# Optimization experiments

Measured on AMD Instinct MI355X. Metric: run time of the kernel, lower is better.

## Reference

```python
import jax, jax.numpy as jnp
import numpy as np

B, N, E, H = 2, 512, 128, 256
IN_DIM = 3 * E + 1


def setup_inputs() -> dict:
    key = jax.random.key(0)
    ks = jax.random.split(key, 9)
    node_embed = jax.random.normal(ks[0], (B, N, E), dtype=jnp.float32)
    problems = jax.random.uniform(ks[1], (B, N, 4), dtype=jnp.float32)
    euclid = jax.random.uniform(ks[2], (B, N, N), dtype=jnp.float32)
    euclid = 0.5 * (euclid + jnp.swapaxes(euclid, 1, 2))  # symmetric, realistic
    s = 0.02
    W1 = s * jax.random.normal(ks[3], (IN_DIM, H), dtype=jnp.float32)
    b1 = jnp.zeros((H,), jnp.float32)
    W2 = s * jax.random.normal(ks[4], (H, H), dtype=jnp.float32)
    b2 = jnp.zeros((H,), jnp.float32)
    W3 = s * jax.random.normal(ks[5], (H, 1), dtype=jnp.float32)
    b3 = jnp.zeros((1,), jnp.float32)
    return {"node_embed": node_embed, "problems": problems,
            "euclid_distance_matrix": euclid,
            "W1": W1, "b1": b1, "W2": W2, "b2": b2, "W3": W3, "b3": b3}


def _forward(node_embed, euclid, W1, b1, W2, b2, W3, b3):
    b, n, e = node_embed.shape
    hi = jnp.broadcast_to(node_embed[:, :, None, :], (b, n, n, e))
    hj = jnp.broadcast_to(node_embed[:, None, :, :], (b, n, n, e))
    habs = jnp.abs(node_embed[:, :, None, :] - node_embed[:, None, :, :])
    x = jnp.concatenate([hi, hj, habs, euclid[..., None]], axis=-1)  # (B,N,N,3E+1)
    h = jax.nn.relu(jnp.einsum('bijf,fh->bijh', x, W1) + b1)
    h = jax.nn.relu(jnp.einsum('bijh,hg->bijg', h, W2) + b2)
    pred = (jnp.einsum('bijh,ho->bijo', h, W3) + b3)[..., 0]  # (B,N,N)
    pred = 0.5 * (pred + jnp.swapaxes(pred, 1, 2))
    pred = pred * (1.0 - jnp.eye(n, dtype=pred.dtype))  # zero diagonal
    return pred


def reference(node_embed, problems, euclid_distance_matrix, W1, b1, W2, b2, W3, b3):
    # euclid_distance_matrix provided, so `problems` fallback path is unused
    return _forward(node_embed, euclid_distance_matrix, W1, b1, W2, b2, W3, b3)
```

## Files before the change

kernel.cpp:

```cpp
#include <hip/hip_runtime.h>
#include <hip/hip_bf16.h>


#define BN 512
#define EE 128
#define HH 256

typedef __attribute__((ext_vector_type(8)))  short short8;
typedef __attribute__((ext_vector_type(4)))  short short4v;
typedef __attribute__((ext_vector_type(16))) float f32x16;
typedef __attribute__((ext_vector_type(4)))  float f32x4;

static __device__ __forceinline__ unsigned short f2bf(float f) {
    __bf16 h = (__bf16)f;
    return __builtin_bit_cast(unsigned short, h);
}
static __device__ __forceinline__ f32x16 zero16() {
    f32x16 v;
    #pragma unroll
    for (int i = 0; i < 16; ++i) v[i] = 0.f;
    return v;
}
#define MFMA(a, b, c) __builtin_amdgcn_mfma_f32_32x32x16_bf16((a), (b), (c), 0, 0, 0)

__global__ void prep(const float* __restrict__ node, const float* __restrict__ W1,
                     const float* __restrict__ W2, const float* __restrict__ b1,
                     float* __restrict__ PA,
                     unsigned short* __restrict__ w1c_p, unsigned short* __restrict__ w1b_p,
                     unsigned short* __restrict__ w2_p,  unsigned short* __restrict__ w1d_f) {
    int blk = blockIdx.x;
    if (blk < 256) {
        int idx = blk * 256 + threadIdx.x;
        {
            int t = idx & 7, l = (idx >> 3) & 63, mt = (idx >> 9) & 7, kb = idx >> 12;
            int k = kb * 16 + (l >> 5) * 8 + t, m = mt * 32 + (l & 31);
            w2_p[idx] = f2bf(W2[k * HH + m]);
            if (idx < 32768) {
                w1c_p[idx] = f2bf(W1[(2 * EE + k) * HH + m]);
                w1b_p[idx] = f2bf(W1[(EE + k) * HH + m]);
            }
        }
        if (idx < 4096) {
            int t = idx & 7, l = (idx >> 3) & 63, mt = idx >> 9;
            int m = mt * 32 + (l & 31);
            bool nz = (t == 0 && l < 32);
            w1d_f[idx] = nz ? f2bf(W1[(3 * EE) * HH + m]) : (unsigned short)0;
        }
    } else {
        int bi = blk - 256;
        int h = threadIdx.x;
        const float* nd = node + (size_t)bi * EE;
        float sa = b1[h];
        #pragma unroll 8
        for (int e = 0; e < EE; ++e) sa += nd[e] * W1[e * HH + h];
        PA[bi * HH + h] = sa;
    }
}

__global__ __launch_bounds__(256, 2) void edge_main(
    const float* __restrict__ node, const float* __restrict__ euclid,
    const float* __restrict__ W3, const float* __restrict__ b3,
    const float* __restrict__ b2v, const float* __restrict__ PA,
    const unsigned short* __restrict__ w1c_p, const unsigned short* __restrict__ w1b_p,
    const unsigned short* __restrict__ w2_p,  const unsigned short* __restrict__ w1d_f,
    float* __restrict__ out)
{
    __shared__ __align__(16) unsigned short lds_buf[2 * 128 * 136];
    __shared__ float pp[512];

    const int jt = blockIdx.x, i = blockIdx.y, b = blockIdx.z;
    const int jbase = jt * 128;
    const int tid = threadIdx.x, wave = tid >> 6, lane = tid & 63;
    const int m0 = lane & 31, q = lane >> 5;

    unsigned short* ldsD  = lds_buf;
    unsigned short* ldsHJ = lds_buf + 128 * 136;
    unsigned short* ldsH1 = lds_buf;

    {
        int row = tid >> 1, half = tid & 1;
        const f32x4* nj = (const f32x4*)(node + ((size_t)b * BN + jbase + row) * EE);
        const f32x4* hv = (const f32x4*)(node + ((size_t)b * BN + i) * EE);
        #pragma unroll
        for (int g = 0; g < 8; ++g) {
            int c0 = half * 16 + g * 2;
            f32x4 a0 = nj[c0], a1 = nj[c0 + 1];
            f32x4 h0 = hv[c0], h1v = hv[c0 + 1];
            short8 pd, ph;
            #pragma unroll
            for (int u = 0; u < 4; ++u) {
                pd[u]     = (short)f2bf(fabsf(a0[u] - h0[u]));
                pd[4 + u] = (short)f2bf(fabsf(a1[u] - h1v[u]));
                ph[u]     = (short)f2bf(a0[u]);
                ph[4 + u] = (short)f2bf(a1[u]);
            }
            int off = row * 136 + half * 64 + g * 8;
            *(short8*)&ldsD[off]  = pd;
            *(short8*)&ldsHJ[off] = ph;
        }
    }
    __syncthreads();

    f32x16 acc[2][4];
    #pragma unroll
    for (int mt = 0; mt < 2; ++mt)
        #pragma unroll
        for (int nt = 0; nt < 4; ++nt) acc[mt][nt] = zero16();
    {
        const short8* wc = (const short8*)w1c_p;
        const short8* wb = (const short8*)w1b_p;
        const int mtg = wave * 2;
        #pragma unroll
        for (int kb = 0; kb < 8; ++kb) {
            short8 ac0 = wc[(kb * 8 + mtg + 0) * 64 + lane];
            short8 ac1 = wc[(kb * 8 + mtg + 1) * 64 + lane];
            short8 ab0 = wb[(kb * 8 + mtg + 0) * 64 + lane];
            short8 ab1 = wb[(kb * 8 + mtg + 1) * 64 + lane];
            #pragma unroll
            for (int nt = 0; nt < 4; ++nt) {
                int off = (nt * 32 + m0) * 136 + kb * 16 + q * 8;
                short8 bD  = *(const short8*)&ldsD[off];
                short8 bHJ = *(const short8*)&ldsHJ[off];
                acc[0][nt] = MFMA(ac0, bD, acc[0][nt]);
                acc[1][nt] = MFMA(ac1, bD, acc[1][nt]);
                acc[0][nt] = MFMA(ab0, bHJ, acc[0][nt]);
                acc[1][nt] = MFMA(ab1, bHJ, acc[1][nt]);
            }
        }
        const float* erow = euclid + ((size_t)b * BN + i) * BN + jbase;
        short8 aw0 = ((const short8*)w1d_f)[(mtg + 0) * 64 + lane];
        short8 aw1 = ((const short8*)w1d_f)[(mtg + 1) * 64 + lane];
        #pragma unroll
        for (int nt = 0; nt < 4; ++nt) {
            short8 be;
            #pragma unroll
            for (int u = 0; u < 8; ++u) be[u] = 0;
            if (lane < 32) be[0] = (short)f2bf(erow[nt * 32 + m0]);
            acc[0][nt] = MFMA(aw0, be, acc[0][nt]);
            acc[1][nt] = MFMA(aw1, be, acc[1][nt]);
        }
    }
    __syncthreads();

    {
        const float* paB = PA + ((size_t)b * BN + i) * HH;
        #pragma unroll
        for (int mt = 0; mt < 2; ++mt) {
            #pragma unroll
            for (int rg = 0; rg < 4; ++rg) {
                int f0 = wave * 64 + mt * 32 + rg * 8;
                f32x4 plo = *(const f32x4*)&paB[f0];
                f32x4 phi = *(const f32x4*)&paB[f0 + 4];
                f32x4 pav;
                #pragma unroll
                for (int u = 0; u < 4; ++u) pav[u] = q ? phi[u] : plo[u];
                #pragma unroll
                for (int nt = 0; nt < 4; ++nt) {
                    short4v w;
                    #pragma unroll
                    for (int u = 0; u < 4; ++u) {
                        float v = acc[mt][nt][rg * 4 + u] + pav[u];
                        v = v > 0.f ? v : 0.f;
                        w[u] = (short)f2bf(v);
                    }
                    *(short4v*)&ldsH1[(nt * 32 + m0) * 264 + f0 + 4 * q] = w;
                }
            }
        }
    }
    __syncthreads();

    f32x16 c2[2][4];
    #pragma unroll
    for (int mt = 0; mt < 2; ++mt)
        #pragma unroll
        for (int nt = 0; nt < 4; ++nt) c2[mt][nt] = zero16();
    {
        const short8* w2f = (const short8*)w2_p;
        const int mtg = wave * 2;
        #pragma unroll
        for (int kb = 0; kb < 16; ++kb) {
            short8 a0 = w2f[(kb * 8 + mtg + 0) * 64 + lane];
            short8 a1 = w2f[(kb * 8 + mtg + 1) * 64 + lane];
            #pragma unroll
            for (int nt = 0; nt < 4; ++nt) {
                short8 bh = *(const short8*)&ldsH1[(nt * 32 + m0) * 264 + kb * 16 + q * 8];
                c2[0][nt] = MFMA(a0, bh, c2[0][nt]);
                c2[1][nt] = MFMA(a1, bh, c2[1][nt]);
            }
        }
    }

    {
        float s[4] = {0.f, 0.f, 0.f, 0.f};
        #pragma unroll
        for (int mt = 0; mt < 2; ++mt) {
            #pragma unroll
            for (int rg = 0; rg < 4; ++rg) {
                int f0 = wave * 64 + mt * 32 + rg * 8;
                f32x4 blo = *(const f32x4*)&b2v[f0];
                f32x4 bhi = *(const f32x4*)&b2v[f0 + 4];
                f32x4 wlo = *(const f32x4*)&W3[f0];
                f32x4 whi = *(const f32x4*)&W3[f0 + 4];
                #pragma unroll
                for (int u = 0; u < 4; ++u) {
                    float bb = q ? bhi[u] : blo[u];
                    float ww = q ? whi[u] : wlo[u];
                    #pragma unroll
                    for (int nt = 0; nt < 4; ++nt) {
                        float h2 = c2[mt][nt][rg * 4 + u] + bb;
                        h2 = h2 > 0.f ? h2 : 0.f;
                        s[nt] += h2 * ww;
                    }
                }
            }
        }
        #pragma unroll
        for (int nt = 0; nt < 4; ++nt)
            s[nt] += __shfl_xor(s[nt], 32, 64);
        if (lane < 32) {
            #pragma unroll
            for (int nt = 0; nt < 4; ++nt)
                pp[wave * 128 + nt * 32 + lane] = s[nt];
        }
    }
    __syncthreads();
    if (tid < 128) {
        float v = pp[tid] + pp[128 + tid] + pp[256 + tid] + pp[384 + tid] + b3[0];
        out[((size_t)b * BN + i) * BN + jbase + tid] = v;
    }
}

__global__ void symmetrize(float* __restrict__ out) {
    int b = blockIdx.z, ti = blockIdx.y, tj = blockIdx.x;
    if (tj < ti) return;
    int i = ti * 32 + threadIdx.y, j = tj * 32 + threadIdx.x;
    float* p = out + (size_t)b * BN * BN;
    if (i == j) { p[(size_t)i * BN + j] = 0.f; return; }
    if (j < i) return;
    float a = p[(size_t)i * BN + j];
    float c = p[(size_t)j * BN + i];
    float v = 0.5f * (a + c);
    p[(size_t)i * BN + j] = v;
    p[(size_t)j * BN + i] = v;
}

extern "C" void kernel_launch(void* const* d_in, const int* in_sizes, int n_in,
                              void* d_out, int out_size, void* d_ws, size_t ws_size,
                              hipStream_t stream) {
    const float* node   = (const float*)d_in[0];
    const float* euclid = (const float*)d_in[2];
    const float* W1     = (const float*)d_in[3];
    const float* b1     = (const float*)d_in[4];
    const float* W2     = (const float*)d_in[5];
    const float* b2     = (const float*)d_in[6];
    const float* W3     = (const float*)d_in[7];
    const float* b3     = (const float*)d_in[8];
    float* out = (float*)d_out;

    char* ws = (char*)d_ws;
    float*          PA    = (float*)ws;
    unsigned short* w1c_p = (unsigned short*)(ws + (1u << 20));
    unsigned short* w1b_p = (unsigned short*)(ws + (1u << 20) + 65536);
    unsigned short* w2_p  = (unsigned short*)(ws + (1u << 20) + 131072);
    unsigned short* w1d_f = (unsigned short*)(ws + (1u << 20) + 262144);

    prep<<<1280, 256, 0, stream>>>(node, W1, W2, b1, PA, w1c_p, w1b_p, w2_p, w1d_f);
    edge_main<<<dim3(BN / 128, BN, 2), 256, 0, stream>>>(
        node, euclid, W3, b3, b2, PA, w1c_p, w1b_p, w2_p, w1d_f, out);
    symmetrize<<<dim3(BN / 32, BN / 32, 2), dim3(32, 32), 0, stream>>>(out);
}
```

Measured before the change: 236.1 us.

## Persistent 512-thread blocks loop over 16 rows with double-buffered diff tiles

The edge kernel now launches 256 blocks of 512 threads, and each block iterates over 16 consecutive i rows for a fixed 128-column j tile. The hj bf16 tile is staged in LDS once per block. The |hi-hj| tile for the next row is computed into a second LDS buffer during the current row's first-layer MFMAs, and the output store for the previous row is deferred into the next iteration. The aim is to amortise per-block staging and launch overhead and to overlap global loads with compute. In exchange the grid is much smaller, LDS use per block is larger, and each wave handles a 2x2 tile subset.

```diff
diff --git a/kernel.cpp b/kernel.cpp
--- a/kernel.cpp
+++ b/kernel.cpp
@@ -57,7 +57,7 @@
     }
 }
 
-__global__ __launch_bounds__(256, 2) void edge_main(
+__global__ __launch_bounds__(512, 2) void edge_main(
     const float* __restrict__ node, const float* __restrict__ euclid,
     const float* __restrict__ W3, const float* __restrict__ b3,
     const float* __restrict__ b2v, const float* __restrict__ PA,
@@ -65,27 +65,36 @@
     const unsigned short* __restrict__ w2_p,  const unsigned short* __restrict__ w1d_f,
     float* __restrict__ out)
 {
-    __shared__ __align__(16) unsigned short lds_buf[2 * 128 * 136];
+    __shared__ __align__(16) unsigned short Rd[2][128 * 136];
+    __shared__ __align__(16) unsigned short Rh[128 * 136];
+    __shared__ __align__(16) unsigned short Rhj[128 * 136];
     __shared__ float pp[512];
 
-    const int jt = blockIdx.x, i = blockIdx.y, b = blockIdx.z;
-    const int jbase = jt * 128;
+    const int wg = blockIdx.x;
+    const int b = wg >> 7, jt = (wg >> 5) & 3, ig = wg & 31;
+    const int jbase = jt * 128, i0 = ig * 16;
     const int tid = threadIdx.x, wave = tid >> 6, lane = tid & 63;
     const int m0 = lane & 31, q = lane >> 5;
-
-    unsigned short* ldsD  = lds_buf;
-    unsigned short* ldsHJ = lds_buf + 128 * 136;
-    unsigned short* ldsH1 = lds_buf;
+    const int mt2 = wave & 3, ntg = wave >> 2;
+    const int nt0 = 2 * ntg, nt1 = 2 * ntg + 1;
+
+    const int brow = tid >> 2, bq4 = tid & 3;
+    const f32x4* njp = (const f32x4*)(node + ((size_t)b * BN + jbase + brow) * EE);
+
+    const float b3v = b3[0];
+    const short8 aw0 = ((const short8*)w1d_f)[(2 * mt2 + 0) * 64 + lane];
+    const short8 aw1 = ((const short8*)w1d_f)[(2 * mt2 + 1) * 64 + lane];
+    const short8* wc  = (const short8*)w1c_p;
+    const short8* wb  = (const short8*)w1b_p;
+    const short8* w2f = (const short8*)w2_p;
 
     {
-        int row = tid >> 1, half = tid & 1;
-        const f32x4* nj = (const f32x4*)(node + ((size_t)b * BN + jbase + row) * EE);
-        const f32x4* hv = (const f32x4*)(node + ((size_t)b * BN + i) * EE);
+        const f32x4* hv = (const f32x4*)(node + ((size_t)b * BN + i0) * EE);
         #pragma unroll
-        for (int g = 0; g < 8; ++g) {
-            int c0 = half * 16 + g * 2;
-            f32x4 a0 = nj[c0], a1 = nj[c0 + 1];
-            f32x4 h0 = hv[c0], h1v = hv[c0 + 1];
+        for (int k = 0; k < 4; ++k) {
+            int c0 = bq4 * 8 + k * 2;
+            f32x4 a0 = njp[c0], a1 = njp[c0 + 1];
+            f32x4 h0 = hv[c0],  h1v = hv[c0 + 1];
             short8 pd, ph;
             #pragma unroll
             for (int u = 0; u < 4; ++u) {
@@ -94,140 +103,154 @@
                 ph[u]     = (short)f2bf(a0[u]);
                 ph[4 + u] = (short)f2bf(a1[u]);
             }
-            int off = row * 136 + half * 64 + g * 8;
-            *(short8*)&ldsD[off]  = pd;
-            *(short8*)&ldsHJ[off] = ph;
+            int off = brow * 136 + bq4 * 32 + k * 8;
+            *(short8*)&Rd[0][off]  = pd;
+            *(short8*)&Rhj[off]    = ph;
         }
     }
     __syncthreads();
 
-    f32x16 acc[2][4];
-    #pragma unroll
-    for (int mt = 0; mt < 2; ++mt)
-        #pragma unroll
-        for (int nt = 0; nt < 4; ++nt) acc[mt][nt] = zero16();
-    {
-        const short8* wc = (const short8*)w1c_p;
-        const short8* wb = (const short8*)w1b_p;
-        const int mtg = wave * 2;
-        #pragma unroll
-        for (int kb = 0; kb < 8; ++kb) {
-            short8 ac0 = wc[(kb * 8 + mtg + 0) * 64 + lane];
-            short8 ac1 = wc[(kb * 8 + mtg + 1) * 64 + lane];
-            short8 ab0 = wb[(kb * 8 + mtg + 0) * 64 + lane];
-            short8 ab1 = wb[(kb * 8 + mtg + 1) * 64 + lane];
-            #pragma unroll
-            for (int nt = 0; nt < 4; ++nt) {
-                int off = (nt * 32 + m0) * 136 + kb * 16 + q * 8;
-                short8 bD  = *(const short8*)&ldsD[off];
-                short8 bHJ = *(const short8*)&ldsHJ[off];
-                acc[0][nt] = MFMA(ac0, bD, acc[0][nt]);
-                acc[1][nt] = MFMA(ac1, bD, acc[1][nt]);
-                acc[0][nt] = MFMA(ab0, bHJ, acc[0][nt]);
-                acc[1][nt] = MFMA(ab1, bHJ, acc[1][nt]);
-            }
-        }
-        const float* erow = euclid + ((size_t)b * BN + i) * BN + jbase;
-        short8 aw0 = ((const short8*)w1d_f)[(mtg + 0) * 64 + lane];
-        short8 aw1 = ((const short8*)w1d_f)[(mtg + 1) * 64 + lane];
-        #pragma unroll
-        for (int nt = 0; nt < 4; ++nt) {
-            short8 be;
-            #pragma unroll
-            for (int u = 0; u < 8; ++u) be[u] = 0;
-            if (lane < 32) be[0] = (short)f2bf(erow[nt * 32 + m0]);
-            acc[0][nt] = MFMA(aw0, be, acc[0][nt]);
-            acc[1][nt] = MFMA(aw1, be, acc[1][nt]);
-        }
-    }
-    __syncthreads();
-
-    {
-        const float* paB = PA + ((size_t)b * BN + i) * HH;
-        #pragma unroll
-        for (int mt = 0; mt < 2; ++mt) {
-            #pragma unroll
-            for (int rg = 0; rg < 4; ++rg) {
-                int f0 = wave * 64 + mt * 32 + rg * 8;
-                f32x4 plo = *(const f32x4*)&paB[f0];
-                f32x4 phi = *(const f32x4*)&paB[f0 + 4];
-                f32x4 pav;
-                #pragma unroll
-                for (int u = 0; u < 4; ++u) pav[u] = q ? phi[u] : plo[u];
-                #pragma unroll
-                for (int nt = 0; nt < 4; ++nt) {
-                    short4v w;
+    #pragma unroll 1
+    for (int tt = 0; tt < 16; ++tt) {
+        const int i = i0 + tt;
+        unsigned short* Dcur = Rd[tt & 1];
+        unsigned short* Dnxt = Rd[(tt + 1) & 1];
+
+        if (tt > 0 && tid < 128) {
+            float v = pp[tid * 4] + pp[tid * 4 + 1] + pp[tid * 4 + 2] + pp[tid * 4 + 3] + b3v;
+            out[((size_t)b * BN + (i - 1)) * BN + jbase + tid] = v;
+        }
+
+        f32x16 acc[2][2];
+        acc[0][0] = zero16(); acc[0][1] = zero16();
+        acc[1][0] = zero16(); acc[1][1] = zero16();
+        {
+            const f32x4* hvn = (const f32x4*)(node + ((size_t)b * BN + i + 1) * EE);
+            #pragma unroll
+            for (int kb = 0; kb < 8; ++kb) {
+                if (kb < 4 && tt < 15) {
+                    int c0 = bq4 * 8 + kb * 2;
+                    f32x4 a0 = njp[c0], a1 = njp[c0 + 1];
+                    f32x4 h0 = hvn[c0], h1v = hvn[c0 + 1];
+                    short8 pd;
                     #pragma unroll
                     for (int u = 0; u < 4; ++u) {
-                        float v = acc[mt][nt][rg * 4 + u] + pav[u];
-                        v = v > 0.f ? v : 0.f;
-                        w[u] = (short)f2bf(v);
+                        pd[u]     = (short)f2bf(fabsf(a0[u] - h0[u]));
+                        pd[4 + u] = (short)f2bf(fabsf(a1[u] - h1v[u]));
                     }
-                    *(short4v*)&ldsH1[(nt * 32 + m0) * 264 + f0 + 4 * q] = w;
+                    *(short8*)&Dnxt[brow * 136 + bq4 * 32 + kb * 8] = pd;
                 }
-            }
-        }
-    }
-    __syncthreads();
-
-    f32x16 c2[2][4];
-    #pragma unroll
-    for (int mt = 0; mt < 2; ++mt)
-        #pragma unroll
-        for (int nt = 0; nt < 4; ++nt) c2[mt][nt] = zero16();
-    {
-        const short8* w2f = (const short8*)w2_p;
-        const int mtg = wave * 2;
-        #pragma unroll
-        for (int kb = 0; kb < 16; ++kb) {
-            short8 a0 = w2f[(kb * 8 + mtg + 0) * 64 + lane];
-            short8 a1 = w2f[(kb * 8 + mtg + 1) * 64 + lane];
-            #pragma unroll
-            for (int nt = 0; nt < 4; ++nt) {
-                short8 bh = *(const short8*)&ldsH1[(nt * 32 + m0) * 264 + kb * 16 + q * 8];
-                c2[0][nt] = MFMA(a0, bh, c2[0][nt]);
-                c2[1][nt] = MFMA(a1, bh, c2[1][nt]);
-            }
-        }
-    }
-
-    {
-        float s[4] = {0.f, 0.f, 0.f, 0.f};
-        #pragma unroll
-        for (int mt = 0; mt < 2; ++mt) {
-            #pragma unroll
-            for (int rg = 0; rg < 4; ++rg) {
-                int f0 = wave * 64 + mt * 32 + rg * 8;
-                f32x4 blo = *(const f32x4*)&b2v[f0];
-                f32x4 bhi = *(const f32x4*)&b2v[f0 + 4];
-                f32x4 wlo = *(const f32x4*)&W3[f0];
-                f32x4 whi = *(const f32x4*)&W3[f0 + 4];
+                short8 ac0 = wc[(kb * 8 + 2 * mt2 + 0) * 64 + lane];
+                short8 ac1 = wc[(kb * 8 + 2 * mt2 + 1) * 64 + lane];
+                short8 ab0 = wb[(kb * 8 + 2 * mt2 + 0) * 64 + lane];
+                short8 ab1 = wb[(kb * 8 + 2 * mt2 + 1) * 64 + lane];
+                int o0 = (nt0 * 32 + m0) * 136 + kb * 16 + q * 8;
+                int o1 = (nt1 * 32 + m0) * 136 + kb * 16 + q * 8;
+                short8 bD0 = *(const short8*)&Dcur[o0];
+                short8 bD1 = *(const short8*)&Dcur[o1];
+                short8 bH0 = *(const short8*)&Rhj[o0];
+                short8 bH1 = *(const short8*)&Rhj[o1];
+                acc[0][0] = MFMA(ac0, bD0, acc[0][0]);
+                acc[1][0] = MFMA(ac1, bD0, acc[1][0]);
+                acc[0][1] = MFMA(ac0, bD1, acc[0][1]);
+                acc[1][1] = MFMA(ac1, bD1, acc[1][1]);
+                acc[0][0] = MFMA(ab0, bH0, acc[0][0]);
+                acc[1][0] = MFMA(ab1, bH0, acc[1][0]);
+                acc[0][1] = MFMA(ab0, bH1, acc[0][1]);
+                acc[1][1] = MFMA(ab1, bH1, acc[1][1]);
+            }
+            const float* erow = euclid + ((size_t)b * BN + i) * BN + jbase;
+            #pragma unroll
+            for (int nt2 = 0; nt2 < 2; ++nt2) {
+                short8 be;
                 #pragma unroll
-                for (int u = 0; u < 4; ++u) {
-                    float bb = q ? bhi[u] : blo[u];
-                    float ww = q ? whi[u] : wlo[u];
+                for (int u = 0; u < 8; ++u) be[u] = 0;
+                if (lane < 32) be[0] = (short)f2bf(erow[(nt0 + nt2) * 32 + m0]);
+                acc[0][nt2] = MFMA(aw0, be, acc[0][nt2]);
+                acc[1][nt2] = MFMA(aw1, be, acc[1][nt2]);
+            }
+        }
+        __syncthreads();
+
+        {
+            const float* paB = PA + ((size_t)b * BN + i) * HH;
+            unsigned short* base = (mt2 < 2) ? Dcur : Rh;
+            #pragma unroll
+            for (int mtl = 0; mtl < 2; ++mtl) {
+                int mt = 2 * mt2 + mtl;
+                #pragma unroll
+                for (int rg = 0; rg < 4; ++rg) {
+                    int f0 = mt * 32 + rg * 8 + 4 * q;
+                    f32x4 pav = *(const f32x4*)&paB[f0];
+                    int lc = f0 & 127;
                     #pragma unroll
-                    for (int nt = 0; nt < 4; ++nt) {
-                        float h2 = c2[mt][nt][rg * 4 + u] + bb;
-                        h2 = h2 > 0.f ? h2 : 0.f;
-                        s[nt] += h2 * ww;
+                    for (int nt2 = 0; nt2 < 2; ++nt2) {
+                        short4v w;
+                        #pragma unroll
+                        for (int u = 0; u < 4; ++u) {
+                            float v = acc[mtl][nt2][rg * 4 + u] + pav[u];
+                            v = v > 0.f ? v : 0.f;
+                            w[u] = (short)f2bf(v);
+                        }
+                        *(short4v*)&base[((nt0 + nt2) * 32 + m0) * 136 + lc] = w;
                     }
                 }
             }
         }
-        #pragma unroll
-        for (int nt = 0; nt < 4; ++nt)
-            s[nt] += __shfl_xor(s[nt], 32, 64);
-        if (lane < 32) {
-            #pragma unroll
-            for (int nt = 0; nt < 4; ++nt)
-                pp[wave * 128 + nt * 32 + lane] = s[nt];
-        }
-    }
-    __syncthreads();
+        __syncthreads();
+
+        f32x16 c2[2][2];
+        c2[0][0] = zero16(); c2[0][1] = zero16();
+        c2[1][0] = zero16(); c2[1][1] = zero16();
+        {
+            #pragma unroll
+            for (int kb = 0; kb < 16; ++kb) {
+                const unsigned short* src = (kb < 8) ? Dcur : Rh;
+                short8 a0 = w2f[(kb * 8 + 2 * mt2 + 0) * 64 + lane];
+                short8 a1 = w2f[(kb * 8 + 2 * mt2 + 1) * 64 + lane];
+                int o0 = (nt0 * 32 + m0) * 136 + (kb & 7) * 16 + q * 8;
+                int o1 = (nt1 * 32 + m0) * 136 + (kb & 7) * 16 + q * 8;
+                short8 bh0 = *(const short8*)&src[o0];
+                short8 bh1 = *(const short8*)&src[o1];
+                c2[0][0] = MFMA(a0, bh0, c2[0][0]);
+                c2[1][0] = MFMA(a1, bh0, c2[1][0]);
+                c2[0][1] = MFMA(a0, bh1, c2[0][1]);
+                c2[1][1] = MFMA(a1, bh1, c2[1][1]);
+            }
+        }
+        {
+            float s0 = 0.f, s1 = 0.f;
+            #pragma unroll
+            for (int mtl = 0; mtl < 2; ++mtl) {
+                #pragma unroll
+                for (int rg = 0; rg < 4; ++rg) {
+                    int f0 = (2 * mt2 + mtl) * 32 + rg * 8 + 4 * q;
+                    f32x4 bb = *(const f32x4*)&b2v[f0];
+                    f32x4 ww = *(const f32x4*)&W3[f0];
+                    #pragma unroll
+                    for (int u = 0; u < 4; ++u) {
+                        float h2a = c2[mtl][0][rg * 4 + u] + bb[u];
+                        h2a = h2a > 0.f ? h2a : 0.f;
+                        s0 += h2a * ww[u];
+                        float h2b = c2[mtl][1][rg * 4 + u] + bb[u];
+                        h2b = h2b > 0.f ? h2b : 0.f;
+                        s1 += h2b * ww[u];
+                    }
+                }
+            }
+            s0 += __shfl_xor(s0, 32, 64);
+            s1 += __shfl_xor(s1, 32, 64);
+            if (lane < 32) {
+                pp[(nt0 * 32 + lane) * 4 + mt2] = s0;
+                pp[(nt1 * 32 + lane) * 4 + mt2] = s1;
+            }
+        }
+        __syncthreads();
+    }
+
     if (tid < 128) {
-        float v = pp[tid] + pp[128 + tid] + pp[256 + tid] + pp[384 + tid] + b3[0];
-        out[((size_t)b * BN + i) * BN + jbase + tid] = v;
+        float v = pp[tid * 4] + pp[tid * 4 + 1] + pp[tid * 4 + 2] + pp[tid * 4 + 3] + b3v;
+        out[((size_t)b * BN + (i0 + 15)) * BN + jbase + tid] = v;
     }
 }
 
@@ -266,7 +289,7 @@
     unsigned short* w1d_f = (unsigned short*)(ws + (1u << 20) + 262144);
 
     prep<<<1280, 256, 0, stream>>>(node, W1, W2, b1, PA, w1c_p, w1b_p, w2_p, w1d_f);
-    edge_main<<<dim3(BN / 128, BN, 2), 256, 0, stream>>>(
+    edge_main<<<256, 512, 0, stream>>>(
         node, euclid, W3, b3, b2, PA, w1c_p, w1b_p, w2_p, w1d_f, out);
     symmetrize<<<dim3(BN / 32, BN / 32, 2), dim3(32, 32), 0, stream>>>(out);
 }
```

Result: slower. 455.9 us (+93.1%).

## Precompute hj·W1 per node and loop eight i rows per block

Applied to the files above, without the earlier changes.

The hj contribution to layer 1 is now computed once per node in the prep kernel as PB, a per-node projection, and loaded to initialise the accumulators. This removes half of the layer-1 MFMAs and the hj LDS staging. The edge kernel becomes a 512-block grid where each block processes eight consecutive i rows in a loop. This is meant to amortise per-block setup and weight fetches, at the cost of fewer blocks in flight and extra fp32 global reads of PB per iteration. An empty asm barrier stops the compiler from hoisting the loop-invariant loads and blowing up register use.

```diff
diff --git a/kernel.cpp b/kernel.cpp
--- a/kernel.cpp
+++ b/kernel.cpp
@@ -25,9 +25,9 @@
 
 __global__ void prep(const float* __restrict__ node, const float* __restrict__ W1,
                      const float* __restrict__ W2, const float* __restrict__ b1,
-                     float* __restrict__ PA,
-                     unsigned short* __restrict__ w1c_p, unsigned short* __restrict__ w1b_p,
-                     unsigned short* __restrict__ w2_p,  unsigned short* __restrict__ w1d_f) {
+                     float* __restrict__ PA, float* __restrict__ PB,
+                     unsigned short* __restrict__ w1c_p, unsigned short* __restrict__ w2_p,
+                     unsigned short* __restrict__ w1d_f) {
     int blk = blockIdx.x;
     if (blk < 256) {
         int idx = blk * 256 + threadIdx.x;
@@ -35,10 +35,8 @@
             int t = idx & 7, l = (idx >> 3) & 63, mt = (idx >> 9) & 7, kb = idx >> 12;
             int k = kb * 16 + (l >> 5) * 8 + t, m = mt * 32 + (l & 31);
             w2_p[idx] = f2bf(W2[k * HH + m]);
-            if (idx < 32768) {
+            if (idx < 32768)
                 w1c_p[idx] = f2bf(W1[(2 * EE + k) * HH + m]);
-                w1b_p[idx] = f2bf(W1[(EE + k) * HH + m]);
-            }
         }
         if (idx < 4096) {
             int t = idx & 7, l = (idx >> 3) & 63, mt = idx >> 9;
@@ -50,10 +48,15 @@
         int bi = blk - 256;
         int h = threadIdx.x;
         const float* nd = node + (size_t)bi * EE;
-        float sa = b1[h];
-        #pragma unroll 8
-        for (int e = 0; e < EE; ++e) sa += nd[e] * W1[e * HH + h];
+        float sa = b1[h], sb = 0.f;
+        #pragma unroll 4
+        for (int e = 0; e < EE; ++e) {
+            float x = nd[e];
+            sa += x * W1[e * HH + h];
+            sb += x * W1[(EE + e) * HH + h];
+        }
         PA[bi * HH + h] = sa;
+        PB[bi * HH + h] = sb;
     }
 }
 
@@ -61,173 +64,179 @@
     const float* __restrict__ node, const float* __restrict__ euclid,
     const float* __restrict__ W3, const float* __restrict__ b3,
     const float* __restrict__ b2v, const float* __restrict__ PA,
-    const unsigned short* __restrict__ w1c_p, const unsigned short* __restrict__ w1b_p,
-    const unsigned short* __restrict__ w2_p,  const unsigned short* __restrict__ w1d_f,
+    const float* __restrict__ PB,
+    const unsigned short* __restrict__ w1c_p, const unsigned short* __restrict__ w2_p,
+    const unsigned short* __restrict__ w1d_f,
     float* __restrict__ out)
 {
-    __shared__ __align__(16) unsigned short lds_buf[2 * 128 * 136];
+    __shared__ __align__(16) unsigned short lds_buf[128 * 264];
     __shared__ float pp[512];
 
-    const int jt = blockIdx.x, i = blockIdx.y, b = blockIdx.z;
-    const int jbase = jt * 128;
+    const int id = blockIdx.x;
+    const int ig = id >> 3, b = (id >> 2) & 1, jt = id & 3;
+    const int jbase = jt * 128, i0 = ig * 8;
     const int tid = threadIdx.x, wave = tid >> 6, lane = tid & 63;
     const int m0 = lane & 31, q = lane >> 5;
-
-    unsigned short* ldsD  = lds_buf;
-    unsigned short* ldsHJ = lds_buf + 128 * 136;
-    unsigned short* ldsH1 = lds_buf;
-
-    {
-        int row = tid >> 1, half = tid & 1;
-        const f32x4* nj = (const f32x4*)(node + ((size_t)b * BN + jbase + row) * EE);
-        const f32x4* hv = (const f32x4*)(node + ((size_t)b * BN + i) * EE);
+    const int brow = tid >> 1, bhalf = tid & 1;
+
+    const float b3v = b3[0];
+    const short8 aw0 = ((const short8*)w1d_f)[(wave * 2 + 0) * 64 + lane];
+    const short8 aw1 = ((const short8*)w1d_f)[(wave * 2 + 1) * 64 + lane];
+    const float* pbBase = PB + ((size_t)b * BN + jbase) * HH;
+    int prow[4];
+    #pragma unroll
+    for (int nt = 0; nt < 4; ++nt) prow[nt] = (nt * 32 + m0) * HH;
+
+    #pragma unroll 1
+    for (int tt = 0; tt < 8; ++tt) {
+        const int i = i0 + tt;
+        size_t z = 0;
+        asm volatile("" : "+s"(z));
+        const short8* wcT = (const short8*)w1c_p + z;
+        const short8* w2T = (const short8*)w2_p + z;
+        const float*  pbT = pbBase + z;
+        const f32x4*  njT = (const f32x4*)(node + ((size_t)b * BN + jbase + brow) * EE) + z;
+        const float*  b2T = b2v + z;
+        const float*  w3T = W3 + z;
+
+        f32x16 acc[2][4];
         #pragma unroll
-        for (int g = 0; g < 8; ++g) {
-            int c0 = half * 16 + g * 2;
-            f32x4 a0 = nj[c0], a1 = nj[c0 + 1];
-            f32x4 h0 = hv[c0], h1v = hv[c0 + 1];
-            short8 pd, ph;
-            #pragma unroll
-            for (int u = 0; u < 4; ++u) {
-                pd[u]     = (short)f2bf(fabsf(a0[u] - h0[u]));
-                pd[4 + u] = (short)f2bf(fabsf(a1[u] - h1v[u]));
-                ph[u]     = (short)f2bf(a0[u]);
-                ph[4 + u] = (short)f2bf(a1[u]);
-            }
-            int off = row * 136 + half * 64 + g * 8;
-            *(short8*)&ldsD[off]  = pd;
-            *(short8*)&ldsHJ[off] = ph;
-        }
-    }
-    __syncthreads();
-
-    f32x16 acc[2][4];
-    #pragma unroll
-    for (int mt = 0; mt < 2; ++mt)
+        for (int mtl = 0; mtl < 2; ++mtl) {
+            #pragma unroll
+            for (int rg = 0; rg < 4; ++rg) {
+                int f0 = wave * 64 + mtl * 32 + rg * 8 + 4 * q;
+                #pragma unroll
+                for (int nt = 0; nt < 4; ++nt) {
+                    f32x4 v = *(const f32x4*)&pbT[prow[nt] + f0];
+                    #pragma unroll
+                    for (int u = 0; u < 4; ++u) acc[mtl][nt][rg * 4 + u] = v[u];
+                }
+            }
+        }
+        const float* erow = euclid + ((size_t)b * BN + i) * BN + jbase;
+        float ev[4];
         #pragma unroll
-        for (int nt = 0; nt < 4; ++nt) acc[mt][nt] = zero16();
-    {
-        const short8* wc = (const short8*)w1c_p;
-        const short8* wb = (const short8*)w1b_p;
-        const int mtg = wave * 2;
+        for (int nt = 0; nt < 4; ++nt) ev[nt] = erow[nt * 32 + m0];
+
+        {
+            const f32x4* hv = (const f32x4*)(node + ((size_t)b * BN + i) * EE);
+            #pragma unroll
+            for (int g = 0; g < 8; ++g) {
+                int c0 = bhalf * 16 + g * 2;
+                f32x4 a0 = njT[c0], a1 = njT[c0 + 1];
+                f32x4 h0 = hv[c0],  h1v = hv[c0 + 1];
+                short8 pd;
+                #pragma unroll
+                for (int u = 0; u < 4; ++u) {
+                    pd[u]     = (short)f2bf(fabsf(a0[u] - h0[u]));
+                    pd[4 + u] = (short)f2bf(fabsf(a1[u] - h1v[u]));
+                }
+                *(short8*)&lds_buf[brow * 136 + bhalf * 64 + g * 8] = pd;
+            }
+        }
+        __syncthreads();
+
+        {
+            #pragma unroll
+            for (int kb = 0; kb < 8; ++kb) {
+                short8 ac0 = wcT[(kb * 8 + wave * 2 + 0) * 64 + lane];
+                short8 ac1 = wcT[(kb * 8 + wave * 2 + 1) * 64 + lane];
+                #pragma unroll
+                for (int nt = 0; nt < 4; ++nt) {
+                    short8 bD = *(const short8*)&lds_buf[(nt * 32 + m0) * 136 + kb * 16 + q * 8];
+                    acc[0][nt] = MFMA(ac0, bD, acc[0][nt]);
+                    acc[1][nt] = MFMA(ac1, bD, acc[1][nt]);
+                }
+            }
+            #pragma unroll
+            for (int nt = 0; nt < 4; ++nt) {
+                short8 be;
+                #pragma unroll
+                for (int u = 0; u < 8; ++u) be[u] = 0;
+                if (lane < 32) be[0] = (short)f2bf(ev[nt]);
+                acc[0][nt] = MFMA(aw0, be, acc[0][nt]);
+                acc[1][nt] = MFMA(aw1, be, acc[1][nt]);
+            }
+        }
+        __syncthreads();
+
+        {
+            const float* paB = PA + ((size_t)b * BN + i) * HH;
+            #pragma unroll
+            for (int mtl = 0; mtl < 2; ++mtl) {
+                #pragma unroll
+                for (int rg = 0; rg < 4; ++rg) {
+                    int f0 = wave * 64 + mtl * 32 + rg * 8 + 4 * q;
+                    f32x4 pav = *(const f32x4*)&paB[f0];
+                    #pragma unroll
+                    for (int nt = 0; nt < 4; ++nt) {
+                        short4v w;
+                        #pragma unroll
+                        for (int u = 0; u < 4; ++u) {
+                            float v = acc[mtl][nt][rg * 4 + u] + pav[u];
+                            v = v > 0.f ? v : 0.f;
+                            w[u] = (short)f2bf(v);
+                        }
+                        *(short4v*)&lds_buf[(nt * 32 + m0) * 264 + f0] = w;
+                    }
+                }
+            }
+        }
+        __syncthreads();
+
+        f32x16 c2[2][4];
         #pragma unroll
-        for (int kb = 0; kb < 8; ++kb) {
-            short8 ac0 = wc[(kb * 8 + mtg + 0) * 64 + lane];
-            short8 ac1 = wc[(kb * 8 + mtg + 1) * 64 + lane];
-            short8 ab0 = wb[(kb * 8 + mtg + 0) * 64 + lane];
-            short8 ab1 = wb[(kb * 8 + mtg + 1) * 64 + lane];
-            #pragma unroll
-            for (int nt = 0; nt < 4; ++nt) {
-                int off = (nt * 32 + m0) * 136 + kb * 16 + q * 8;
-                short8 bD  = *(const short8*)&ldsD[off];
-                short8 bHJ = *(const short8*)&ldsHJ[off];
-                acc[0][nt] = MFMA(ac0, bD, acc[0][nt]);
-                acc[1][nt] = MFMA(ac1, bD, acc[1][nt]);
-                acc[0][nt] = MFMA(ab0, bHJ, acc[0][nt]);
-                acc[1][nt] = MFMA(ab1, bHJ, acc[1][nt]);
-            }
-        }
-        const float* erow = euclid + ((size_t)b * BN + i) * BN + jbase;
-        short8 aw0 = ((const short8*)w1d_f)[(mtg + 0) * 64 + lane];
-        short8 aw1 = ((const short8*)w1d_f)[(mtg + 1) * 64 + lane];
-        #pragma unroll
-        for (int nt = 0; nt < 4; ++nt) {
-            short8 be;
-            #pragma unroll
-            for (int u = 0; u < 8; ++u) be[u] = 0;
-            if (lane < 32) be[0] = (short)f2bf(erow[nt * 32 + m0]);
-            acc[0][nt] = MFMA(aw0, be, acc[0][nt]);
-            acc[1][nt] = MFMA(aw1, be, acc[1][nt]);
-        }
-    }
-    __syncthreads();
-
-    {
-        const float* paB = PA + ((size_t)b * BN + i) * HH;
-        #pragma unroll
-        for (int mt = 0; mt < 2; ++mt) {
-            #pragma unroll
-            for (int rg = 0; rg < 4; ++rg) {
-                int f0 = wave * 64 + mt * 32 + rg * 8;
-                f32x4 plo = *(const f32x4*)&paB[f0];
-                f32x4 phi = *(const f32x4*)&paB[f0 + 4];
-                f32x4 pav;
-                #pragma unroll
-                for (int u = 0; u < 4; ++u) pav[u] = q ? phi[u] : plo[u];
+        for (int mtl = 0; mtl < 2; ++mtl)
+            #pragma unroll
+            for (int nt = 0; nt < 4; ++nt) c2[mtl][nt] = zero16();
+        {
+            #pragma unroll
+            for (int kb = 0; kb < 16; ++kb) {
+                short8 a0 = w2T[(kb * 8 + wave * 2 + 0) * 64 + lane];
+                short8 a1 = w2T[(kb * 8 + wave * 2 + 1) * 64 + lane];
                 #pragma unroll
                 for (int nt = 0; nt < 4; ++nt) {
-                    short4v w;
+                    short8 bh = *(const short8*)&lds_buf[(nt * 32 + m0) * 264 + kb * 16 + q * 8];
+                    c2[0][nt] = MFMA(a0, bh, c2[0][nt]);
+                    c2[1][nt] = MFMA(a1, bh, c2[1][nt]);
+                }
+            }
+        }
+
+        {
+            float s[4] = {0.f, 0.f, 0.f, 0.f};
+            #pragma unroll
+            for (int mtl = 0; mtl < 2; ++mtl) {
+                #pragma unroll
+                for (int rg = 0; rg < 4; ++rg) {
+                    int f0 = wave * 64 + mtl * 32 + rg * 8 + 4 * q;
+                    f32x4 bb = *(const f32x4*)&b2T[f0];
+                    f32x4 ww = *(const f32x4*)&w3T[f0];
                     #pragma unroll
                     for (int u = 0; u < 4; ++u) {
-                        float v = acc[mt][nt][rg * 4 + u] + pav[u];
-                        v = v > 0.f ? v : 0.f;
-                        w[u] = (short)f2bf(v);
+                        #pragma unroll
+                        for (int nt = 0; nt < 4; ++nt) {
+                            float h2 = c2[mtl][nt][rg * 4 + u] + bb[u];
+                            h2 = h2 > 0.f ? h2 : 0.f;
+                            s[nt] += h2 * ww[u];
+                        }
                     }
-                    *(short4v*)&ldsH1[(nt * 32 + m0) * 264 + f0 + 4 * q] = w;
-                }
-            }
-        }
-    }
-    __syncthreads();
-
-    f32x16 c2[2][4];
-    #pragma unroll
-    for (int mt = 0; mt < 2; ++mt)
-        #pragma unroll
-        for (int nt = 0; nt < 4; ++nt) c2[mt][nt] = zero16();
-    {
-        const short8* w2f = (const short8*)w2_p;
-        const int mtg = wave * 2;
-        #pragma unroll
-        for (int kb = 0; kb < 16; ++kb) {
-            short8 a0 = w2f[(kb * 8 + mtg + 0) * 64 + lane];
-            short8 a1 = w2f[(kb * 8 + mtg + 1) * 64 + lane];
-            #pragma unroll
-            for (int nt = 0; nt < 4; ++nt) {
-                short8 bh = *(const short8*)&ldsH1[(nt * 32 + m0) * 264 + kb * 16 + q * 8];
-                c2[0][nt] = MFMA(a0, bh, c2[0][nt]);
-                c2[1][nt] = MFMA(a1, bh, c2[1][nt]);
-            }
-        }
-    }
-
-    {
-        float s[4] = {0.f, 0.f, 0.f, 0.f};
-        #pragma unroll
-        for (int mt = 0; mt < 2; ++mt) {
-            #pragma unroll
-            for (int rg = 0; rg < 4; ++rg) {
-                int f0 = wave * 64 + mt * 32 + rg * 8;
-                f32x4 blo = *(const f32x4*)&b2v[f0];
-                f32x4 bhi = *(const f32x4*)&b2v[f0 + 4];
-                f32x4 wlo = *(const f32x4*)&W3[f0];
-                f32x4 whi = *(const f32x4*)&W3[f0 + 4];
-                #pragma unroll
-                for (int u = 0; u < 4; ++u) {
-                    float bb = q ? bhi[u] : blo[u];
-                    float ww = q ? whi[u] : wlo[u];
-                    #pragma unroll
-                    for (int nt = 0; nt < 4; ++nt) {
-                        float h2 = c2[mt][nt][rg * 4 + u] + bb;
-                        h2 = h2 > 0.f ? h2 : 0.f;
-                        s[nt] += h2 * ww;
-                    }
-                }
-            }
-        }
-        #pragma unroll
-        for (int nt = 0; nt < 4; ++nt)
-            s[nt] += __shfl_xor(s[nt], 32, 64);
-        if (lane < 32) {
+                }
+            }
             #pragma unroll
             for (int nt = 0; nt < 4; ++nt)
-                pp[wave * 128 + nt * 32 + lane] = s[nt];
-        }
-    }
-    __syncthreads();
-    if (tid < 128) {
-        float v = pp[tid] + pp[128 + tid] + pp[256 + tid] + pp[384 + tid] + b3[0];
-        out[((size_t)b * BN + i) * BN + jbase + tid] = v;
+                s[nt] += __shfl_xor(s[nt], 32, 64);
+            if (lane < 32) {
+                #pragma unroll
+                for (int nt = 0; nt < 4; ++nt)
+                    pp[wave * 128 + nt * 32 + lane] = s[nt];
+            }
+        }
+        __syncthreads();
+        if (tid < 128) {
+            float v = pp[tid] + pp[128 + tid] + pp[256 + tid] + pp[384 + tid] + b3v;
+            out[((size_t)b * BN + i) * BN + jbase + tid] = v;
+        }
     }
 }
 
@@ -260,13 +269,13 @@
 
     char* ws = (char*)d_ws;
     float*          PA    = (float*)ws;
-    unsigned short* w1c_p = (unsigned short*)(ws + (1u << 20));
-    unsigned short* w1b_p = (unsigned short*)(ws + (1u << 20) + 65536);
-    unsigned short* w2_p  = (unsigned short*)(ws + (1u << 20) + 131072);
-    unsigned short* w1d_f = (unsigned short*)(ws + (1u << 20) + 262144);
-
-    prep<<<1280, 256, 0, stream>>>(node, W1, W2, b1, PA, w1c_p, w1b_p, w2_p, w1d_f);
-    edge_main<<<dim3(BN / 128, BN, 2), 256, 0, stream>>>(
-        node, euclid, W3, b3, b2, PA, w1c_p, w1b_p, w2_p, w1d_f, out);
+    float*          PB    = (float*)(ws + (1u << 20));
+    unsigned short* w1c_p = (unsigned short*)(ws + (2u << 20));
+    unsigned short* w2_p  = (unsigned short*)(ws + (2u << 20) + 65536);
+    unsigned short* w1d_f = (unsigned short*)(ws + (2u << 20) + 196608);
+
+    prep<<<1280, 256, 0, stream>>>(node, W1, W2, b1, PA, PB, w1c_p, w2_p, w1d_f);
+    edge_main<<<512, 256, 0, stream>>>(
+        node, euclid, W3, b3, b2, PA, PB, w1c_p, w2_p, w1d_f, out);
     symmetrize<<<dim3(BN / 32, BN / 32, 2), dim3(32, 32), 0, stream>>>(out);
 }
```

Measured after the change: 270.7 us. 1.15x slower.

## Loop each edge block over eight rows and stagger waves by hardware ID

Applied to the files above, without the earlier changes.

The edge kernel grid shrinks from 4096 blocks to 512 persistent-style blocks. Each block loops over 8 consecutive i rows for a fixed j tile and batch, and hoists the w1d fragments and b3 out of that loop. An empty asm offset keeps weight loads from being hoisted or merged across iterations, and the PA, b2 and W3 loads become single 16-byte reads per lane. Blocks on odd hardware IDs sleep at start, which looks like an attempt to stagger MFMA and memory phases across CUs. The sleep adds fixed latency, and the smaller grid may reduce latency hiding.

```diff
diff --git a/kernel.cpp b/kernel.cpp
--- a/kernel.cpp
+++ b/kernel.cpp
@@ -68,166 +68,180 @@
     __shared__ __align__(16) unsigned short lds_buf[2 * 128 * 136];
     __shared__ float pp[512];
 
-    const int jt = blockIdx.x, i = blockIdx.y, b = blockIdx.z;
-    const int jbase = jt * 128;
+    {
+        int hwid = 0;
+        asm volatile("s_getreg_b32 %0, hwreg(HW_REG_HW_ID, 0, 4)" : "=s"(hwid));
+        if (hwid & 1) {
+            __builtin_amdgcn_s_sleep(127);
+            __builtin_amdgcn_s_sleep(127);
+            __builtin_amdgcn_s_sleep(127);
+        }
+    }
+
+    const int id = blockIdx.x;
+    const int jt = id & 3, b = (id >> 2) & 1, ig = id >> 3;
+    const int jbase = jt * 128, i0 = ig * 8;
     const int tid = threadIdx.x, wave = tid >> 6, lane = tid & 63;
     const int m0 = lane & 31, q = lane >> 5;
+    const int brow = tid >> 1, bhalf = tid & 1;
 
     unsigned short* ldsD  = lds_buf;
     unsigned short* ldsHJ = lds_buf + 128 * 136;
     unsigned short* ldsH1 = lds_buf;
 
-    {
-        int row = tid >> 1, half = tid & 1;
-        const f32x4* nj = (const f32x4*)(node + ((size_t)b * BN + jbase + row) * EE);
-        const f32x4* hv = (const f32x4*)(node + ((size_t)b * BN + i) * EE);
+    const float b3v = b3[0];
+    const short8 aw0 = ((const short8*)w1d_f)[(wave * 2 + 0) * 64 + lane];
+    const short8 aw1 = ((const short8*)w1d_f)[(wave * 2 + 1) * 64 + lane];
+
+    #pragma unroll 1
+    for (int tt = 0; tt < 8; ++tt) {
+        const int i = i0 + tt;
+        size_t z = 0;
+        asm volatile("" : "+s"(z));
+        const short8* wcT = (const short8*)w1c_p + z;
+        const short8* wbT = (const short8*)w1b_p + z;
+        const short8* w2T = (const short8*)w2_p + z;
+        const f32x4*  njT = (const f32x4*)(node + ((size_t)b * BN + jbase + brow) * EE) + z;
+        const float*  b2T = b2v + z;
+        const float*  w3T = W3 + z;
+
+        {
+            const f32x4* hv = (const f32x4*)(node + ((size_t)b * BN + i) * EE);
+            #pragma unroll
+            for (int g = 0; g < 8; ++g) {
+                int c0 = bhalf * 16 + g * 2;
+                f32x4 a0 = njT[c0], a1 = njT[c0 + 1];
+                f32x4 h0 = hv[c0],  h1v = hv[c0 + 1];
+                short8 pd, ph;
+                #pragma unroll
+                for (int u = 0; u < 4; ++u) {
+                    pd[u]     = (short)f2bf(fabsf(a0[u] - h0[u]));
+                    pd[4 + u] = (short)f2bf(fabsf(a1[u] - h1v[u]));
+                    ph[u]     = (short)f2bf(a0[u]);
+                    ph[4 + u] = (short)f2bf(a1[u]);
+                }
+                int off = brow * 136 + bhalf * 64 + g * 8;
+                *(short8*)&ldsD[off]  = pd;
+                *(short8*)&ldsHJ[off] = ph;
+            }
+        }
+        __syncthreads();
+
+        f32x16 acc[2][4];
         #pragma unroll
-        for (int g = 0; g < 8; ++g) {
-            int c0 = half * 16 + g * 2;
-            f32x4 a0 = nj[c0], a1 = nj[c0 + 1];
-            f32x4 h0 = hv[c0], h1v = hv[c0 + 1];
-            short8 pd, ph;
-            #pragma unroll
-            for (int u = 0; u < 4; ++u) {
-                pd[u]     = (short)f2bf(fabsf(a0[u] - h0[u]));
-                pd[4 + u] = (short)f2bf(fabsf(a1[u] - h1v[u]));
-                ph[u]     = (short)f2bf(a0[u]);
-                ph[4 + u] = (short)f2bf(a1[u]);
-            }
-            int off = row * 136 + half * 64 + g * 8;
-            *(short8*)&ldsD[off]  = pd;
-            *(short8*)&ldsHJ[off] = ph;
-        }
-    }
-    __syncthreads();
-
-    f32x16 acc[2][4];
-    #pragma unroll
-    for (int mt = 0; mt < 2; ++mt)
+        for (int mt = 0; mt < 2; ++mt)
+            #pragma unroll
+            for (int nt = 0; nt < 4; ++nt) acc[mt][nt] = zero16();
+        {
+            const int mtg = wave * 2;
+            #pragma unroll
+            for (int kb = 0; kb < 8; ++kb) {
+                short8 ac0 = wcT[(kb * 8 + mtg + 0) * 64 + lane];
+                short8 ac1 = wcT[(kb * 8 + mtg + 1) * 64 + lane];
+                short8 ab0 = wbT[(kb * 8 + mtg + 0) * 64 + lane];
+                short8 ab1 = wbT[(kb * 8 + mtg + 1) * 64 + lane];
+                #pragma unroll
+                for (int nt = 0; nt < 4; ++nt) {
+                    int off = (nt * 32 + m0) * 136 + kb * 16 + q * 8;
+                    short8 bD  = *(const short8*)&ldsD[off];
+                    short8 bHJ = *(const short8*)&ldsHJ[off];
+                    acc[0][nt] = MFMA(ac0, bD, acc[0][nt]);
+                    acc[1][nt] = MFMA(ac1, bD, acc[1][nt]);
+                    acc[0][nt] = MFMA(ab0, bHJ, acc[0][nt]);
+                    acc[1][nt] = MFMA(ab1, bHJ, acc[1][nt]);
+                }
+            }
+            const float* erow = euclid + ((size_t)b * BN + i) * BN + jbase;
+            #pragma unroll
+            for (int nt = 0; nt < 4; ++nt) {
+                short8 be;
+                #pragma unroll
+                for (int u = 0; u < 8; ++u) be[u] = 0;
+                if (lane < 32) be[0] = (short)f2bf(erow[nt * 32 + m0]);
+                acc[0][nt] = MFMA(aw0, be, acc[0][nt]);
+                acc[1][nt] = MFMA(aw1, be, acc[1][nt]);
+            }
+        }
+        __syncthreads();
+
+        {
+            const float* paB = PA + ((size_t)b * BN + i) * HH;
+            #pragma unroll
+            for (int mt = 0; mt < 2; ++mt) {
+                #pragma unroll
+                for (int rg = 0; rg < 4; ++rg) {
+                    int f0 = wave * 64 + mt * 32 + rg * 8 + 4 * q;
+                    f32x4 pav = *(const f32x4*)&paB[f0];
+                    #pragma unroll
+                    for (int nt = 0; nt < 4; ++nt) {
+                        short4v w;
+                        #pragma unroll
+                        for (int u = 0; u < 4; ++u) {
+                            float v = acc[mt][nt][rg * 4 + u] + pav[u];
+                            v = v > 0.f ? v : 0.f;
+                            w[u] = (short)f2bf(v);
+                        }
+                        *(short4v*)&ldsH1[(nt * 32 + m0) * 264 + f0] = w;
+                    }
+                }
+            }
+        }
+        __syncthreads();
+
+        f32x16 c2[2][4];
         #pragma unroll
-        for (int nt = 0; nt < 4; ++nt) acc[mt][nt] = zero16();
-    {
-        const short8* wc = (const short8*)w1c_p;
-        const short8* wb = (const short8*)w1b_p;
-        const int mtg = wave * 2;
-        #pragma unroll
-        for (int kb = 0; kb < 8; ++kb) {
-            short8 ac0 = wc[(kb * 8 + mtg + 0) * 64 + lane];
-            short8 ac1 = wc[(kb * 8 + mtg + 1) * 64 + lane];
-            short8 ab0 = wb[(kb * 8 + mtg + 0) * 64 + lane];
-            short8 ab1 = wb[(kb * 8 + mtg + 1) * 64 + lane];
-            #pragma unroll
-            for (int nt = 0; nt < 4; ++nt) {
-                int off = (nt * 32 + m0) * 136 + kb * 16 + q * 8;
-                short8 bD  = *(const short8*)&ldsD[off];
-                short8 bHJ = *(const short8*)&ldsHJ[off];
-                acc[0][nt] = MFMA(ac0, bD, acc[0][nt]);
-                acc[1][nt] = MFMA(ac1, bD, acc[1][nt]);
-                acc[0][nt] = MFMA(ab0, bHJ, acc[0][nt]);
-                acc[1][nt] = MFMA(ab1, bHJ, acc[1][nt]);
-            }
-        }
-        const float* erow = euclid + ((size_t)b * BN + i) * BN + jbase;
-        short8 aw0 = ((const short8*)w1d_f)[(mtg + 0) * 64 + lane];
-        short8 aw1 = ((const short8*)w1d_f)[(mtg + 1) * 64 + lane];
-        #pragma unroll
-        for (int nt = 0; nt < 4; ++nt) {
-            short8 be;
-            #pragma unroll
-            for (int u = 0; u < 8; ++u) be[u] = 0;
-            if (lane < 32) be[0] = (short)f2bf(erow[nt * 32 + m0]);
-            acc[0][nt] = MFMA(aw0, be, acc[0][nt]);
-            acc[1][nt] = MFMA(aw1, be, acc[1][nt]);
-        }
-    }
-    __syncthreads();
-
-    {
-        const float* paB = PA + ((size_t)b * BN + i) * HH;
-        #pragma unroll
-        for (int mt = 0; mt < 2; ++mt) {
-            #pragma unroll
-            for (int rg = 0; rg < 4; ++rg) {
-                int f0 = wave * 64 + mt * 32 + rg * 8;
-                f32x4 plo = *(const f32x4*)&paB[f0];
-                f32x4 phi = *(const f32x4*)&paB[f0 + 4];
-                f32x4 pav;
-                #pragma unroll
-                for (int u = 0; u < 4; ++u) pav[u] = q ? phi[u] : plo[u];
+        for (int mt = 0; mt < 2; ++mt)
+            #pragma unroll
+            for (int nt = 0; nt < 4; ++nt) c2[mt][nt] = zero16();
+        {
+            const int mtg = wave * 2;
+            #pragma unroll
+            for (int kb = 0; kb < 16; ++kb) {
+                short8 a0 = w2T[(kb * 8 + mtg + 0) * 64 + lane];
+                short8 a1 = w2T[(kb * 8 + mtg + 1) * 64 + lane];
                 #pragma unroll
                 for (int nt = 0; nt < 4; ++nt) {
-                    short4v w;
+                    short8 bh = *(const short8*)&ldsH1[(nt * 32 + m0) * 264 + kb * 16 + q * 8];
+                    c2[0][nt] = MFMA(a0, bh, c2[0][nt]);
+                    c2[1][nt] = MFMA(a1, bh, c2[1][nt]);
+                }
+            }
+        }
+
+        {
+            float s[4] = {0.f, 0.f, 0.f, 0.f};
+            #pragma unroll
+            for (int mt = 0; mt < 2; ++mt) {
+                #pragma unroll
+                for (int rg = 0; rg < 4; ++rg) {
+                    int f0 = wave * 64 + mt * 32 + rg * 8 + 4 * q;
+                    f32x4 bb = *(const f32x4*)&b2T[f0];
+                    f32x4 ww = *(const f32x4*)&w3T[f0];
                     #pragma unroll
                     for (int u = 0; u < 4; ++u) {
-                        float v = acc[mt][nt][rg * 4 + u] + pav[u];
-                        v = v > 0.f ? v : 0.f;
-                        w[u] = (short)f2bf(v);
+                        #pragma unroll
+                        for (int nt = 0; nt < 4; ++nt) {
+                            float h2 = c2[mt][nt][rg * 4 + u] + bb[u];
+                            h2 = h2 > 0.f ? h2 : 0.f;
+                            s[nt] += h2 * ww[u];
+                        }
                     }
-                    *(short4v*)&ldsH1[(nt * 32 + m0) * 264 + f0 + 4 * q] = w;
-                }
-            }
-        }
-    }
-    __syncthreads();
-
-    f32x16 c2[2][4];
-    #pragma unroll
-    for (int mt = 0; mt < 2; ++mt)
-        #pragma unroll
-        for (int nt = 0; nt < 4; ++nt) c2[mt][nt] = zero16();
-    {
-        const short8* w2f = (const short8*)w2_p;
-        const int mtg = wave * 2;
-        #pragma unroll
-        for (int kb = 0; kb < 16; ++kb) {
-            short8 a0 = w2f[(kb * 8 + mtg + 0) * 64 + lane];
-            short8 a1 = w2f[(kb * 8 + mtg + 1) * 64 + lane];
-            #pragma unroll
-            for (int nt = 0; nt < 4; ++nt) {
-                short8 bh = *(const short8*)&ldsH1[(nt * 32 + m0) * 264 + kb * 16 + q * 8];
-                c2[0][nt] = MFMA(a0, bh, c2[0][nt]);
-                c2[1][nt] = MFMA(a1, bh, c2[1][nt]);
-            }
-        }
-    }
-
-    {
-        float s[4] = {0.f, 0.f, 0.f, 0.f};
-        #pragma unroll
-        for (int mt = 0; mt < 2; ++mt) {
-            #pragma unroll
-            for (int rg = 0; rg < 4; ++rg) {
-                int f0 = wave * 64 + mt * 32 + rg * 8;
-                f32x4 blo = *(const f32x4*)&b2v[f0];
-                f32x4 bhi = *(const f32x4*)&b2v[f0 + 4];
-                f32x4 wlo = *(const f32x4*)&W3[f0];
-                f32x4 whi = *(const f32x4*)&W3[f0 + 4];
-                #pragma unroll
-                for (int u = 0; u < 4; ++u) {
-                    float bb = q ? bhi[u] : blo[u];
-                    float ww = q ? whi[u] : wlo[u];
-                    #pragma unroll
-                    for (int nt = 0; nt < 4; ++nt) {
-                        float h2 = c2[mt][nt][rg * 4 + u] + bb;
-                        h2 = h2 > 0.f ? h2 : 0.f;
-                        s[nt] += h2 * ww;
-                    }
-                }
-            }
-        }
-        #pragma unroll
-        for (int nt = 0; nt < 4; ++nt)
-            s[nt] += __shfl_xor(s[nt], 32, 64);
-        if (lane < 32) {
+                }
+            }
             #pragma unroll
             for (int nt = 0; nt < 4; ++nt)
-                pp[wave * 128 + nt * 32 + lane] = s[nt];
-        }
-    }
-    __syncthreads();
-    if (tid < 128) {
-        float v = pp[tid] + pp[128 + tid] + pp[256 + tid] + pp[384 + tid] + b3[0];
-        out[((size_t)b * BN + i) * BN + jbase + tid] = v;
+                s[nt] += __shfl_xor(s[nt], 32, 64);
+            if (lane < 32) {
+                #pragma unroll
+                for (int nt = 0; nt < 4; ++nt)
+                    pp[wave * 128 + nt * 32 + lane] = s[nt];
+            }
+        }
+        __syncthreads();
+        if (tid < 128) {
+            float v = pp[tid] + pp[128 + tid] + pp[256 + tid] + pp[384 + tid] + b3v;
+            out[((size_t)b * BN + i) * BN + jbase + tid] = v;
+        }
     }
 }
 
@@ -266,7 +280,7 @@
     unsigned short* w1d_f = (unsigned short*)(ws + (1u << 20) + 262144);
 
     prep<<<1280, 256, 0, stream>>>(node, W1, W2, b1, PA, w1c_p, w1b_p, w2_p, w1d_f);
-    edge_main<<<dim3(BN / 128, BN, 2), 256, 0, stream>>>(
+    edge_main<<<512, 256, 0, stream>>>(
         node, euclid, W3, b3, b2, PA, w1c_p, w1b_p, w2_p, w1d_f, out);
     symmetrize<<<dim3(BN / 32, BN / 32, 2), dim3(32, 32), 0, stream>>>(out);
 }
```

Result: slower. 251.5 us (+6.5%).
